# Kernel tuning notes

Hardware: AMD Instinct MI355X
Metric: run time of the kernel (lower is better)

## Reference

```python
import jax, jax.numpy as jnp
import numpy as np

B, I, O = 32768, 512, 512
EPS = 1e-5


def setup_inputs() -> dict:
    key = jax.random.key(0)
    ks = jax.random.split(key, 4)
    return {
        "input": jax.random.normal(ks[0], (B, I), dtype=jnp.float32),
        "h": jax.random.normal(ks[1], (B, O), dtype=jnp.float32),
        "c": jax.random.normal(ks[2], (B, O), dtype=jnp.float32),
        "W": jax.random.normal(ks[3], (4 * O, I + O), dtype=jnp.float32) * (1.0 / np.sqrt(I + O)),
        "gamma": jnp.ones((4, O), dtype=jnp.float32),
        "beta": jnp.zeros((4, O), dtype=jnp.float32),
    }


def reference(input, h, c, W, gamma, beta):
    # fused input projection: [B, I+O] @ [I+O, 4O] -> [B, 4, O]
    z = jnp.einsum("bi,gi->bg", jnp.concatenate([input, h], axis=-1), W)
    z = z.reshape(z.shape[0], 4, O)
    # LayerNorm over the trailing [4, O] dims jointly (torch LayerNorm([x, o_size]))
    mean = jnp.mean(z, axis=(-2, -1), keepdims=True)
    var = jnp.var(z, axis=(-2, -1), keepdims=True)
    zn = (z - mean) * jax.lax.rsqrt(var + EPS) * gamma + beta
    f_gate = jax.nn.sigmoid(zn[:, 0])
    i_gate = jax.nn.sigmoid(zn[:, 1])
    o_gate = jax.nn.sigmoid(zn[:, 2])
    # GELU (torch default = exact erf); dropout is identity in eval mode
    h_state = jax.nn.gelu(zn[:, 3], approximate=False)
    cell = f_gate * c + i_gate * h_state
    output = o_gate * cell
    return (output, cell)
```

## Files before the change

### kernel.cpp

```cpp
#include <hip/hip_runtime.h>
#include <hip/hip_bf16.h>
#include <cstdint>
#include <cstddef>

#define BDIM 32768
#define IDIM 512
#define ODIM 512
#define KDIM 1024
#define NDIM 2048

typedef __attribute__((ext_vector_type(8))) __bf16 bf16x8;
typedef __attribute__((ext_vector_type(4))) float f32x4;
typedef __attribute__((ext_vector_type(8))) unsigned short u16x8;

__device__ __forceinline__ unsigned short f2bf(float x) {
  union { float f; uint32_t u; } v; v.f = x;
  uint32_t r = v.u + 0x7FFFu + ((v.u >> 16) & 1u);
  return (unsigned short)(r >> 16);
}

__device__ __forceinline__ float bf2f(unsigned short s) {
  union { uint32_t u; float f; } v; v.u = ((uint32_t)s) << 16;
  return v.f;
}


__global__ __launch_bounds__(256) void pack_a_kernel(const float* __restrict__ in,
                                                     const float* __restrict__ h,
                                                     unsigned short* __restrict__ A) {
  size_t t = (size_t)blockIdx.x * 256 + threadIdx.x;
  size_t e = t * 8;
  size_t b = e >> 10;
  int col = (int)(e & 1023);
  const float* src = (col < IDIM) ? (in + b * IDIM + col)
                                  : (h + b * ODIM + (col - IDIM));
  float4 v0 = ((const float4*)src)[0];
  float4 v1 = ((const float4*)src)[1];
  u16x8 r;
  r[0] = f2bf(v0.x); r[1] = f2bf(v0.y); r[2] = f2bf(v0.z); r[3] = f2bf(v0.w);
  r[4] = f2bf(v1.x); r[5] = f2bf(v1.y); r[6] = f2bf(v1.z); r[7] = f2bf(v1.w);
  *(u16x8*)(A + e) = r;
}

__global__ __launch_bounds__(256) void pack_w_kernel(const float* __restrict__ Wsrc,
                                                     unsigned short* __restrict__ Wb) {
  size_t t = (size_t)blockIdx.x * 256 + threadIdx.x;
  size_t e = t * 8;
  float4 v0 = ((const float4*)(Wsrc + e))[0];
  float4 v1 = ((const float4*)(Wsrc + e))[1];
  u16x8 r;
  r[0] = f2bf(v0.x); r[1] = f2bf(v0.y); r[2] = f2bf(v0.z); r[3] = f2bf(v0.w);
  r[4] = f2bf(v1.x); r[5] = f2bf(v1.y); r[6] = f2bf(v1.z); r[7] = f2bf(v1.w);
  *(u16x8*)(Wb + e) = r;
}


#define BUFSZ 32768
#define ABYTES 16384

#define BAR() do { asm volatile("" ::: "memory"); __builtin_amdgcn_s_barrier(); asm volatile("" ::: "memory"); } while (0)
#define VMW(n) asm volatile("s_waitcnt vmcnt(" #n ")" ::: "memory")

__device__ __forceinline__ void gll16(const unsigned short* src, char* ldsdst) {
  __builtin_amdgcn_global_load_lds(
      (const __attribute__((address_space(1))) void*)src,
      (__attribute__((address_space(3))) void*)ldsdst, 16, 0, 0);
}

template<int BUF, int VM, bool STG, int TO>
__device__ __forceinline__ void tile_body(char* smem,
                                          const unsigned short* sA0, const unsigned short* sA1,
                                          const unsigned short* sB0, const unsigned short* sB1,
                                          int wave1024, int aoff, int boff,
                                          f32x4 (&acc)[8][4]) {
  char* const Ab = smem + BUF * BUFSZ;
  char* const Bb = Ab + ABYTES;
  constexpr int DB = ((BUF + 3) & 3) * BUFSZ;

  if (VM == 8)      VMW(8);
  else if (VM == 4) VMW(4);
  else              VMW(0);
  BAR();

  bf16x8 x0 = *(const bf16x8*)(Ab + aoff + 0 * 1024);
  bf16x8 x1 = *(const bf16x8*)(Ab + aoff + 1 * 1024);
  bf16x8 x2 = *(const bf16x8*)(Ab + aoff + 2 * 1024);
  bf16x8 x3 = *(const bf16x8*)(Ab + aoff + 3 * 1024);
  bf16x8 b0 = *(const bf16x8*)(Bb + boff + 0 * 1024);
  bf16x8 b1 = *(const bf16x8*)(Bb + boff + 1 * 1024);
  bf16x8 b2 = *(const bf16x8*)(Bb + boff + 2 * 1024);
  bf16x8 b3 = *(const bf16x8*)(Bb + boff + 3 * 1024);
  if (STG) {
    gll16(sA0 + TO * 32, smem + DB + wave1024);
    gll16(sB0 + TO * 32, smem + DB + ABYTES + wave1024);
  }
  BAR();
  __builtin_amdgcn_sched_barrier(0);
  __builtin_amdgcn_s_setprio(1);
  acc[0][0] = __builtin_amdgcn_mfma_f32_16x16x32_bf16(x0, b0, acc[0][0], 0, 0, 0);
  acc[0][1] = __builtin_amdgcn_mfma_f32_16x16x32_bf16(x0, b1, acc[0][1], 0, 0, 0);
  acc[0][2] = __builtin_amdgcn_mfma_f32_16x16x32_bf16(x0, b2, acc[0][2], 0, 0, 0);
  acc[0][3] = __builtin_amdgcn_mfma_f32_16x16x32_bf16(x0, b3, acc[0][3], 0, 0, 0);
  acc[1][0] = __builtin_amdgcn_mfma_f32_16x16x32_bf16(x1, b0, acc[1][0], 0, 0, 0);
  acc[1][1] = __builtin_amdgcn_mfma_f32_16x16x32_bf16(x1, b1, acc[1][1], 0, 0, 0);
  acc[1][2] = __builtin_amdgcn_mfma_f32_16x16x32_bf16(x1, b2, acc[1][2], 0, 0, 0);
  acc[1][3] = __builtin_amdgcn_mfma_f32_16x16x32_bf16(x1, b3, acc[1][3], 0, 0, 0);
  acc[2][0] = __builtin_amdgcn_mfma_f32_16x16x32_bf16(x2, b0, acc[2][0], 0, 0, 0);
  acc[2][1] = __builtin_amdgcn_mfma_f32_16x16x32_bf16(x2, b1, acc[2][1], 0, 0, 0);
  acc[2][2] = __builtin_amdgcn_mfma_f32_16x16x32_bf16(x2, b2, acc[2][2], 0, 0, 0);
  acc[2][3] = __builtin_amdgcn_mfma_f32_16x16x32_bf16(x2, b3, acc[2][3], 0, 0, 0);
  acc[3][0] = __builtin_amdgcn_mfma_f32_16x16x32_bf16(x3, b0, acc[3][0], 0, 0, 0);
  acc[3][1] = __builtin_amdgcn_mfma_f32_16x16x32_bf16(x3, b1, acc[3][1], 0, 0, 0);
  acc[3][2] = __builtin_amdgcn_mfma_f32_16x16x32_bf16(x3, b2, acc[3][2], 0, 0, 0);
  acc[3][3] = __builtin_amdgcn_mfma_f32_16x16x32_bf16(x3, b3, acc[3][3], 0, 0, 0);
  __builtin_amdgcn_s_setprio(0);
  __builtin_amdgcn_sched_barrier(0);
  BAR();

  x0 = *(const bf16x8*)(Ab + aoff + 4 * 1024);
  x1 = *(const bf16x8*)(Ab + aoff + 5 * 1024);
  x2 = *(const bf16x8*)(Ab + aoff + 6 * 1024);
  x3 = *(const bf16x8*)(Ab + aoff + 7 * 1024);
  if (STG) {
    gll16(sA1 + TO * 32, smem + DB + 8192 + wave1024);
    gll16(sB1 + TO * 32, smem + DB + ABYTES + 8192 + wave1024);
  }
  BAR();
  __builtin_amdgcn_sched_barrier(0);
  __builtin_amdgcn_s_setprio(1);
  acc[4][0] = __builtin_amdgcn_mfma_f32_16x16x32_bf16(x0, b0, acc[4][0], 0, 0, 0);
  acc[4][1] = __builtin_amdgcn_mfma_f32_16x16x32_bf16(x0, b1, acc[4][1], 0, 0, 0);
  acc[4][2] = __builtin_amdgcn_mfma_f32_16x16x32_bf16(x0, b2, acc[4][2], 0, 0, 0);
  acc[4][3] = __builtin_amdgcn_mfma_f32_16x16x32_bf16(x0, b3, acc[4][3], 0, 0, 0);
  acc[5][0] = __builtin_amdgcn_mfma_f32_16x16x32_bf16(x1, b0, acc[5][0], 0, 0, 0);
  acc[5][1] = __builtin_amdgcn_mfma_f32_16x16x32_bf16(x1, b1, acc[5][1], 0, 0, 0);
  acc[5][2] = __builtin_amdgcn_mfma_f32_16x16x32_bf16(x1, b2, acc[5][2], 0, 0, 0);
  acc[5][3] = __builtin_amdgcn_mfma_f32_16x16x32_bf16(x1, b3, acc[5][3], 0, 0, 0);
  acc[6][0] = __builtin_amdgcn_mfma_f32_16x16x32_bf16(x2, b0, acc[6][0], 0, 0, 0);
  acc[6][1] = __builtin_amdgcn_mfma_f32_16x16x32_bf16(x2, b1, acc[6][1], 0, 0, 0);
  acc[6][2] = __builtin_amdgcn_mfma_f32_16x16x32_bf16(x2, b2, acc[6][2], 0, 0, 0);
  acc[6][3] = __builtin_amdgcn_mfma_f32_16x16x32_bf16(x2, b3, acc[6][3], 0, 0, 0);
  acc[7][0] = __builtin_amdgcn_mfma_f32_16x16x32_bf16(x3, b0, acc[7][0], 0, 0, 0);
  acc[7][1] = __builtin_amdgcn_mfma_f32_16x16x32_bf16(x3, b1, acc[7][1], 0, 0, 0);
  acc[7][2] = __builtin_amdgcn_mfma_f32_16x16x32_bf16(x3, b2, acc[7][2], 0, 0, 0);
  acc[7][3] = __builtin_amdgcn_mfma_f32_16x16x32_bf16(x3, b3, acc[7][3], 0, 0, 0);
  __builtin_amdgcn_s_setprio(0);
  __builtin_amdgcn_sched_barrier(0);
}

__global__ __launch_bounds__(512, 2) void gemm_kernel(const unsigned short* __restrict__ A,
                                                      const unsigned short* __restrict__ Bt,
                                                      unsigned short* __restrict__ Cz) {
  extern __shared__ char smem[];
  const int tid = threadIdx.x;
  const int wave = tid >> 6;
  const int lane = tid & 63;

  const int bid = blockIdx.x;
  const int swz = (bid & 7) * 128 + (bid >> 3);
  const int m0 = (swz >> 3) * 256;
  const int n0 = (swz & 7) * 256;

  const int wm = (wave >> 2) * 128;
  const int wn = (wave & 3) * 64;
  const int lrow = lane & 15;
  const int cswz16 = (((lane >> 4) ^ (lrow >> 2)) & 3) * 16;
  const int aoff = (wm + lrow) * 64 + cswz16;
  const int boff = (wn + lrow) * 64 + cswz16;
  const int wave1024 = wave * 1024;

  const int r0 = tid >> 2;
  const int r1 = r0 + 128;
  const int c0 = (tid & 3) ^ ((r0 >> 2) & 3);
  const int c1 = (tid & 3) ^ ((r1 >> 2) & 3);
  const unsigned short* sA0 = A  + (size_t)(m0 + r0) * KDIM + c0 * 8;
  const unsigned short* sA1 = A  + (size_t)(m0 + r1) * KDIM + c1 * 8;
  const unsigned short* sB0 = Bt + (size_t)(n0 + r0) * KDIM + c0 * 8;
  const unsigned short* sB1 = Bt + (size_t)(n0 + r1) * KDIM + c1 * 8;

  f32x4 acc[8][4] = {};

  gll16(sA0,      smem + 0 * BUFSZ + wave1024);
  gll16(sB0,      smem + 0 * BUFSZ + ABYTES + wave1024);
  gll16(sA1,      smem + 0 * BUFSZ + 8192 + wave1024);
  gll16(sB1,      smem + 0 * BUFSZ + ABYTES + 8192 + wave1024);
  gll16(sA0 + 32, smem + 1 * BUFSZ + wave1024);
  gll16(sB0 + 32, smem + 1 * BUFSZ + ABYTES + wave1024);
  gll16(sA1 + 32, smem + 1 * BUFSZ + 8192 + wave1024);
  gll16(sB1 + 32, smem + 1 * BUFSZ + ABYTES + 8192 + wave1024);
  gll16(sA0 + 64, smem + 2 * BUFSZ + wave1024);
  gll16(sB0 + 64, smem + 2 * BUFSZ + ABYTES + wave1024);
  gll16(sA1 + 64, smem + 2 * BUFSZ + 8192 + wave1024);
  gll16(sB1 + 64, smem + 2 * BUFSZ + ABYTES + 8192 + wave1024);

  for (int t4 = 0; t4 < 28; t4 += 4) {
    tile_body<0, 8, true, 3>(smem, sA0, sA1, sB0, sB1, wave1024, aoff, boff, acc);
    tile_body<1, 8, true, 4>(smem, sA0, sA1, sB0, sB1, wave1024, aoff, boff, acc);
    tile_body<2, 8, true, 5>(smem, sA0, sA1, sB0, sB1, wave1024, aoff, boff, acc);
    tile_body<3, 8, true, 6>(smem, sA0, sA1, sB0, sB1, wave1024, aoff, boff, acc);
    sA0 += 128; sA1 += 128; sB0 += 128; sB1 += 128;
  }
  tile_body<0, 8, true,  3>(smem, sA0, sA1, sB0, sB1, wave1024, aoff, boff, acc);
  tile_body<1, 8, false, 0>(smem, sA0, sA1, sB0, sB1, wave1024, aoff, boff, acc);
  tile_body<2, 4, false, 0>(smem, sA0, sA1, sB0, sB1, wave1024, aoff, boff, acc);
  tile_body<3, 0, false, 0>(smem, sA0, sA1, sB0, sB1, wave1024, aoff, boff, acc);

#pragma unroll
  for (int mi = 0; mi < 8; ++mi) {
#pragma unroll
    for (int ni = 0; ni < 4; ++ni) {
#pragma unroll
      for (int r = 0; r < 4; ++r) {
        const int row = m0 + wm + mi * 16 + (lane >> 4) * 4 + r;
        const int col = n0 + wn + ni * 16 + lrow;
        Cz[(size_t)row * NDIM + col] = f2bf(acc[mi][ni][r]);
      }
    }
  }
}


__global__ __launch_bounds__(256) void ln_gate_kernel(const unsigned short* __restrict__ z,
                                                      const float* __restrict__ c,
                                                      const float* __restrict__ gamma,
                                                      const float* __restrict__ beta,
                                                      float* __restrict__ out) {
  __shared__ float rowbuf[4][NDIM];
  const int wave = threadIdx.x >> 6;
  const int lane = threadIdx.x & 63;
  const int row = blockIdx.x * 4 + wave;
  const unsigned short* zr = z + (size_t)row * NDIM;

  float s = 0.f, ss = 0.f;
#pragma unroll
  for (int j = 0; j < 4; ++j) {
    const int chunk = j * 64 + lane;
    u16x8 v = *(const u16x8*)(zr + chunk * 8);
    float f[8];
#pragma unroll
    for (int i2 = 0; i2 < 8; ++i2) {
      f[i2] = bf2f(v[i2]);
      s += f[i2];
      ss += f[i2] * f[i2];
    }
    float4* dst = (float4*)&rowbuf[wave][chunk * 8];
    dst[0] = make_float4(f[0], f[1], f[2], f[3]);
    dst[1] = make_float4(f[4], f[5], f[6], f[7]);
  }
#pragma unroll
  for (int off = 32; off > 0; off >>= 1) {
    s += __shfl_xor(s, off, 64);
    ss += __shfl_xor(ss, off, 64);
  }
  const float mean = s * (1.f / (float)NDIM);
  const float var = ss * (1.f / (float)NDIM) - mean * mean;
  const float inv = rsqrtf(var + 1e-5f);

  float* out_o = out + (size_t)row * ODIM;
  float* out_c = out + (size_t)BDIM * ODIM + (size_t)row * ODIM;
  const float* crow = c + (size_t)row * ODIM;

#pragma unroll
  for (int j = 0; j < 8; ++j) {
    const int o = j * 64 + lane;
    float zn[4];
#pragma unroll
    for (int g = 0; g < 4; ++g) {
      float v = (rowbuf[wave][g * ODIM + o] - mean) * inv;
      zn[g] = v * gamma[g * ODIM + o] + beta[g * ODIM + o];
    }
    const float fg = 1.f / (1.f + expf(-zn[0]));
    const float ig = 1.f / (1.f + expf(-zn[1]));
    const float og = 1.f / (1.f + expf(-zn[2]));
    const float x = zn[3];
    const float hs = 0.5f * x * (1.f + erff(x * 0.70710678118654752f));
    const float cc = fg * crow[o] + ig * hs;
    out_c[o] = cc;
    out_o[o] = og * cc;
  }
}


extern "C" void kernel_launch(void* const* d_in, const int* in_sizes, int n_in,
                              void* d_out, int out_size, void* d_ws, size_t ws_size,
                              hipStream_t stream) {
  const float* input = (const float*)d_in[0];
  const float* h     = (const float*)d_in[1];
  const float* c     = (const float*)d_in[2];
  const float* W     = (const float*)d_in[3];
  const float* gamma = (const float*)d_in[4];
  const float* beta  = (const float*)d_in[5];

  unsigned short* A  = (unsigned short*)d_ws;
  unsigned short* Wb = A + (size_t)BDIM * KDIM;
  unsigned short* z  = Wb + (size_t)NDIM * KDIM;
  float* out = (float*)d_out;

  hipFuncSetAttribute((const void*)gemm_kernel,
                      hipFuncAttributeMaxDynamicSharedMemorySize, 131072);

  pack_a_kernel<<<(BDIM * KDIM / 8) / 256, 256, 0, stream>>>(input, h, A);
  pack_w_kernel<<<(NDIM * KDIM / 8) / 256, 256, 0, stream>>>(W, Wb);
  gemm_kernel<<<dim3((BDIM / 256) * (NDIM / 256)), 512, 131072, stream>>>(A, Wb, z);
  ln_gate_kernel<<<BDIM / 4, 256, 0, stream>>>(z, c, gamma, beta, out);
}
```

Before: 271.3 us.

## Fuse fp32-to-bf16 activation packing into GEMM A-tile staging

Removes the separate pack_a kernel. The GEMM now loads fp32 input/h rows into registers, converts them to bf16 and writes them into LDS itself, while B tiles still use direct global-to-LDS loads. This avoids writing and re-reading a 64 MB bf16 A buffer and saves one launch. In exchange, each of the 8 N-tile blocks re-reads and re-converts the same fp32 A rows (twice the bytes of bf16). Register pressure and VALU work inside the pipelined loop also go up, and the prefetch schedule changes from asynchronous waits to register-held loads.

```diff
diff --git a/kernel.cpp b/kernel.cpp
--- a/kernel.cpp
+++ b/kernel.cpp
@@ -24,23 +24,6 @@
   return v.f;
 }
 
-
-__global__ __launch_bounds__(256) void pack_a_kernel(const float* __restrict__ in,
-                                                     const float* __restrict__ h,
-                                                     unsigned short* __restrict__ A) {
-  size_t t = (size_t)blockIdx.x * 256 + threadIdx.x;
-  size_t e = t * 8;
-  size_t b = e >> 10;
-  int col = (int)(e & 1023);
-  const float* src = (col < IDIM) ? (in + b * IDIM + col)
-                                  : (h + b * ODIM + (col - IDIM));
-  float4 v0 = ((const float4*)src)[0];
-  float4 v1 = ((const float4*)src)[1];
-  u16x8 r;
-  r[0] = f2bf(v0.x); r[1] = f2bf(v0.y); r[2] = f2bf(v0.z); r[3] = f2bf(v0.w);
-  r[4] = f2bf(v1.x); r[5] = f2bf(v1.y); r[6] = f2bf(v1.z); r[7] = f2bf(v1.w);
-  *(u16x8*)(A + e) = r;
-}
 
 __global__ __launch_bounds__(256) void pack_w_kernel(const float* __restrict__ Wsrc,
                                                      unsigned short* __restrict__ Wb) {
@@ -60,6 +43,7 @@
 
 #define BAR() do { asm volatile("" ::: "memory"); __builtin_amdgcn_s_barrier(); asm volatile("" ::: "memory"); } while (0)
 #define VMW(n) asm volatile("s_waitcnt vmcnt(" #n ")" ::: "memory")
+#define LGKM0() do { asm volatile("s_waitcnt lgkmcnt(0)" ::: "memory"); __builtin_amdgcn_sched_barrier(0); } while (0)
 
 __device__ __forceinline__ void gll16(const unsigned short* src, char* ldsdst) {
   __builtin_amdgcn_global_load_lds(
@@ -67,19 +51,25 @@
       (__attribute__((address_space(3))) void*)ldsdst, 16, 0, 0);
 }
 
-template<int BUF, int VM, bool STG, int TO>
+__device__ __forceinline__ u16x8 cvt8(float4 lo, float4 hi) {
+  u16x8 w;
+  w[0] = f2bf(lo.x); w[1] = f2bf(lo.y); w[2] = f2bf(lo.z); w[3] = f2bf(lo.w);
+  w[4] = f2bf(hi.x); w[5] = f2bf(hi.y); w[6] = f2bf(hi.z); w[7] = f2bf(hi.w);
+  return w;
+}
+
+template<int BUF, bool STG, bool TVMW>
 __device__ __forceinline__ void tile_body(char* smem,
-                                          const unsigned short* sA0, const unsigned short* sA1,
+                                          const float* qi0, const float* qh0,
+                                          const float* qi1, const float* qh1,
                                           const unsigned short* sB0, const unsigned short* sB1,
-                                          int wave1024, int aoff, int boff,
-                                          f32x4 (&acc)[8][4]) {
+                                          int kstg, int wave1024, int wl16,
+                                          int aoff, int boff, f32x4 (&acc)[8][4]) {
   char* const Ab = smem + BUF * BUFSZ;
   char* const Bb = Ab + ABYTES;
   constexpr int DB = ((BUF + 3) & 3) * BUFSZ;
 
-  if (VM == 8)      VMW(8);
-  else if (VM == 4) VMW(4);
-  else              VMW(0);
+  if (TVMW) VMW(0);
   BAR();
 
   bf16x8 x0 = *(const bf16x8*)(Ab + aoff + 0 * 1024);
@@ -90,9 +80,12 @@
   bf16x8 b1 = *(const bf16x8*)(Bb + boff + 1 * 1024);
   bf16x8 b2 = *(const bf16x8*)(Bb + boff + 2 * 1024);
   bf16x8 b3 = *(const bf16x8*)(Bb + boff + 3 * 1024);
+  float4 al0, al1, ah0, ah1;
   if (STG) {
-    gll16(sA0 + TO * 32, smem + DB + wave1024);
-    gll16(sB0 + TO * 32, smem + DB + ABYTES + wave1024);
+    const float* s0 = (kstg < 512) ? (qi0 + kstg) : (qh0 + (kstg - 512));
+    const float* s1 = (kstg < 512) ? (qi1 + kstg) : (qh1 + (kstg - 512));
+    al0 = ((const float4*)s0)[0]; al1 = ((const float4*)s0)[1];
+    ah0 = ((const float4*)s1)[0]; ah1 = ((const float4*)s1)[1];
   }
   BAR();
   __builtin_amdgcn_sched_barrier(0);
@@ -122,8 +115,10 @@
   x2 = *(const bf16x8*)(Ab + aoff + 6 * 1024);
   x3 = *(const bf16x8*)(Ab + aoff + 7 * 1024);
   if (STG) {
-    gll16(sA1 + TO * 32, smem + DB + 8192 + wave1024);
-    gll16(sB1 + TO * 32, smem + DB + ABYTES + 8192 + wave1024);
+    gll16(sB0, smem + DB + ABYTES + wave1024);
+    gll16(sB1, smem + DB + ABYTES + 8192 + wave1024);
+    *(u16x8*)(smem + DB + wl16)        = cvt8(al0, al1);
+    *(u16x8*)(smem + DB + 8192 + wl16) = cvt8(ah0, ah1);
   }
   BAR();
   __builtin_amdgcn_sched_barrier(0);
@@ -148,7 +143,8 @@
   __builtin_amdgcn_sched_barrier(0);
 }
 
-__global__ __launch_bounds__(512, 2) void gemm_kernel(const unsigned short* __restrict__ A,
+__global__ __launch_bounds__(512, 2) void gemm_kernel(const float* __restrict__ in_,
+                                                      const float* __restrict__ hp,
                                                       const unsigned short* __restrict__ Bt,
                                                       unsigned short* __restrict__ Cz) {
   extern __shared__ char smem[];
@@ -161,49 +157,61 @@
   const int m0 = (swz >> 3) * 256;
   const int n0 = (swz & 7) * 256;
 
-  const int wm = (wave >> 2) * 128;
+  const int wm = (wave >> 1) * 64;
+  const int wmR = (wave >> 2) * 128;
   const int wn = (wave & 3) * 64;
   const int lrow = lane & 15;
   const int cswz16 = (((lane >> 4) ^ (lrow >> 2)) & 3) * 16;
-  const int aoff = (wm + lrow) * 64 + cswz16;
+  const int aoff = (wmR + lrow) * 64 + cswz16;
   const int boff = (wn + lrow) * 64 + cswz16;
   const int wave1024 = wave * 1024;
+  const int wl16 = wave1024 + lane * 16;
 
   const int r0 = tid >> 2;
   const int r1 = r0 + 128;
   const int c0 = (tid & 3) ^ ((r0 >> 2) & 3);
   const int c1 = (tid & 3) ^ ((r1 >> 2) & 3);
-  const unsigned short* sA0 = A  + (size_t)(m0 + r0) * KDIM + c0 * 8;
-  const unsigned short* sA1 = A  + (size_t)(m0 + r1) * KDIM + c1 * 8;
+  const float* qi0 = in_ + (size_t)(m0 + r0) * IDIM + c0 * 8;
+  const float* qh0 = hp  + (size_t)(m0 + r0) * ODIM + c0 * 8;
+  const float* qi1 = in_ + (size_t)(m0 + r1) * IDIM + c1 * 8;
+  const float* qh1 = hp  + (size_t)(m0 + r1) * ODIM + c1 * 8;
   const unsigned short* sB0 = Bt + (size_t)(n0 + r0) * KDIM + c0 * 8;
   const unsigned short* sB1 = Bt + (size_t)(n0 + r1) * KDIM + c1 * 8;
 
   f32x4 acc[8][4] = {};
 
-  gll16(sA0,      smem + 0 * BUFSZ + wave1024);
-  gll16(sB0,      smem + 0 * BUFSZ + ABYTES + wave1024);
-  gll16(sA1,      smem + 0 * BUFSZ + 8192 + wave1024);
-  gll16(sB1,      smem + 0 * BUFSZ + ABYTES + 8192 + wave1024);
-  gll16(sA0 + 32, smem + 1 * BUFSZ + wave1024);
-  gll16(sB0 + 32, smem + 1 * BUFSZ + ABYTES + wave1024);
-  gll16(sA1 + 32, smem + 1 * BUFSZ + 8192 + wave1024);
-  gll16(sB1 + 32, smem + 1 * BUFSZ + ABYTES + 8192 + wave1024);
-  gll16(sA0 + 64, smem + 2 * BUFSZ + wave1024);
-  gll16(sB0 + 64, smem + 2 * BUFSZ + ABYTES + wave1024);
-  gll16(sA1 + 64, smem + 2 * BUFSZ + 8192 + wave1024);
-  gll16(sB1 + 64, smem + 2 * BUFSZ + ABYTES + 8192 + wave1024);
-
-  for (int t4 = 0; t4 < 28; t4 += 4) {
-    tile_body<0, 8, true, 3>(smem, sA0, sA1, sB0, sB1, wave1024, aoff, boff, acc);
-    tile_body<1, 8, true, 4>(smem, sA0, sA1, sB0, sB1, wave1024, aoff, boff, acc);
-    tile_body<2, 8, true, 5>(smem, sA0, sA1, sB0, sB1, wave1024, aoff, boff, acc);
-    tile_body<3, 8, true, 6>(smem, sA0, sA1, sB0, sB1, wave1024, aoff, boff, acc);
-    sA0 += 128; sA1 += 128; sB0 += 128; sB1 += 128;
-  }
-  tile_body<0, 8, true,  3>(smem, sA0, sA1, sB0, sB1, wave1024, aoff, boff, acc);
-  tile_body<1, 8, false, 0>(smem, sA0, sA1, sB0, sB1, wave1024, aoff, boff, acc);
-  tile_body<2, 4, false, 0>(smem, sA0, sA1, sB0, sB1, wave1024, aoff, boff, acc);
-  tile_body<3, 0, false, 0>(smem, sA0, sA1, sB0, sB1, wave1024, aoff, boff, acc);
+#pragma unroll
+  for (int t = 0; t < 3; ++t) {
+    const int k = t * 32;
+    const float* s0 = (k < 512) ? (qi0 + k) : (qh0 + (k - 512));
+    const float* s1 = (k < 512) ? (qi1 + k) : (qh1 + (k - 512));
+    float4 al0 = ((const float4*)s0)[0], al1 = ((const float4*)s0)[1];
+    float4 ah0 = ((const float4*)s1)[0], ah1 = ((const float4*)s1)[1];
+    *(u16x8*)(smem + t * BUFSZ + wl16)        = cvt8(al0, al1);
+    *(u16x8*)(smem + t * BUFSZ + 8192 + wl16) = cvt8(ah0, ah1);
+    gll16(sB0 + k, smem + t * BUFSZ + ABYTES + wave1024);
+    gll16(sB1 + k, smem + t * BUFSZ + ABYTES + 8192 + wave1024);
+  }
+  VMW(0);
+  LGKM0();
+  BAR();
+  sB0 += 96; sB1 += 96;
+  int kstg = 96;
+
+  for (int tt = 0; tt < 7; ++tt) {
+    tile_body<0, true, false>(smem, qi0, qh0, qi1, qh1, sB0, sB1, kstg, wave1024, wl16, aoff, boff, acc);
+    sB0 += 32; sB1 += 32; kstg += 32;
+    tile_body<1, true, false>(smem, qi0, qh0, qi1, qh1, sB0, sB1, kstg, wave1024, wl16, aoff, boff, acc);
+    sB0 += 32; sB1 += 32; kstg += 32;
+    tile_body<2, true, false>(smem, qi0, qh0, qi1, qh1, sB0, sB1, kstg, wave1024, wl16, aoff, boff, acc);
+    sB0 += 32; sB1 += 32; kstg += 32;
+    tile_body<3, true, false>(smem, qi0, qh0, qi1, qh1, sB0, sB1, kstg, wave1024, wl16, aoff, boff, acc);
+    sB0 += 32; sB1 += 32; kstg += 32;
+  }
+  tile_body<0, true,  false>(smem, qi0, qh0, qi1, qh1, sB0, sB1, kstg, wave1024, wl16, aoff, boff, acc);
+  tile_body<1, false, true >(smem, qi0, qh0, qi1, qh1, sB0, sB1, kstg, wave1024, wl16, aoff, boff, acc);
+  tile_body<2, false, false>(smem, qi0, qh0, qi1, qh1, sB0, sB1, kstg, wave1024, wl16, aoff, boff, acc);
+  tile_body<3, false, false>(smem, qi0, qh0, qi1, qh1, sB0, sB1, kstg, wave1024, wl16, aoff, boff, acc);
 
 #pragma unroll
   for (int mi = 0; mi < 8; ++mi) {
@@ -211,12 +219,13 @@
     for (int ni = 0; ni < 4; ++ni) {
 #pragma unroll
       for (int r = 0; r < 4; ++r) {
-        const int row = m0 + wm + mi * 16 + (lane >> 4) * 4 + r;
+        const int row = m0 + wmR + mi * 16 + (lane >> 4) * 4 + r;
         const int col = n0 + wn + ni * 16 + lrow;
         Cz[(size_t)row * NDIM + col] = f2bf(acc[mi][ni][r]);
       }
     }
   }
+  (void)wm;
 }
 
 
@@ -291,16 +300,14 @@
   const float* gamma = (const float*)d_in[4];
   const float* beta  = (const float*)d_in[5];
 
-  unsigned short* A  = (unsigned short*)d_ws;
-  unsigned short* Wb = A + (size_t)BDIM * KDIM;
+  unsigned short* Wb = (unsigned short*)d_ws;
   unsigned short* z  = Wb + (size_t)NDIM * KDIM;
   float* out = (float*)d_out;
 
   hipFuncSetAttribute((const void*)gemm_kernel,
                       hipFuncAttributeMaxDynamicSharedMemorySize, 131072);
 
-  pack_a_kernel<<<(BDIM * KDIM / 8) / 256, 256, 0, stream>>>(input, h, A);
   pack_w_kernel<<<(NDIM * KDIM / 8) / 256, 256, 0, stream>>>(W, Wb);
-  gemm_kernel<<<dim3((BDIM / 256) * (NDIM / 256)), 512, 131072, stream>>>(A, Wb, z);
+  gemm_kernel<<<dim3((BDIM / 256) * (NDIM / 256)), 512, 131072, stream>>>(input, h, Wb, z);
   ln_gate_kernel<<<BDIM / 4, 256, 0, stream>>>(z, c, gamma, beta, out);
 }
```

After: 330.9 us. 1.22x slower.
